# Optimization experiments

Measured on AMD Instinct MI355X. Metric: run time of the kernel, lower is better.

Reference implementation:

```python
import jax, jax.numpy as jnp
import numpy as np

WS = 7          # window_size
N = WS * WS     # 49 tokens per window
DIM = 384
H = 12
HD = DIM // H   # 32
NW = 64         # windows per image (mask leading dim)


def _rel_pos_index():
    coords = np.stack(np.meshgrid(np.arange(WS), np.arange(WS), indexing='ij'))  # (2, WS, WS)
    cf = coords.reshape(2, -1)                      # (2, N)
    rel = cf[:, :, None] - cf[:, None, :]           # (2, N, N)
    rel = rel.transpose(1, 2, 0)                    # (N, N, 2)
    idx = (rel[..., 0] + WS - 1) * (2 * WS - 1) + (rel[..., 1] + WS - 1)
    return jnp.asarray(idx, dtype=jnp.int32)        # (N, N)

REL_IDX = _rel_pos_index()


def setup_inputs() -> dict:
    key = jax.random.key(0)
    ks = jax.random.split(key, 10)
    B_ = 2048
    x = jax.random.normal(ks[0], (B_, N, DIM), dtype=jnp.float32)
    mask = jnp.zeros((NW, N, N), dtype=jnp.float32)
    s = 0.02
    Wq = jax.random.normal(ks[1], (DIM, DIM), jnp.float32) * s
    Wk = jax.random.normal(ks[2], (DIM, DIM), jnp.float32) * s
    Wv = jax.random.normal(ks[3], (DIM, DIM), jnp.float32) * s
    Wp = jax.random.normal(ks[4], (DIM, DIM), jnp.float32) * s
    bq = jnp.zeros((DIM,), jnp.float32)
    bk = jnp.zeros((DIM,), jnp.float32)
    bv = jnp.zeros((DIM,), jnp.float32)
    bp = jnp.zeros((DIM,), jnp.float32)
    table = jax.random.normal(ks[5], ((2 * WS - 1) ** 2, H), jnp.float32) * s
    return {"x": x, "mask": mask, "Wq": Wq, "bq": bq, "Wk": Wk, "bk": bk,
            "Wv": Wv, "bv": bv, "Wp": Wp, "bp": bp, "table": table}


def reference(x, mask, Wq, bq, Wk, bk, Wv, bv, Wp, bp, table):
    b_, n, c = x.shape
    scale = HD ** (-0.5)
    # projections: PyTorch Linear is x @ W.T + b
    q = (x @ Wq.T + bq).reshape(b_, n, H, HD).transpose(0, 2, 1, 3)  # (B, H, N, D)
    k = (x @ Wk.T + bk).reshape(b_, n, H, HD).transpose(0, 2, 1, 3)
    v = (x @ Wv.T + bv).reshape(b_, n, H, HD).transpose(0, 2, 1, 3)
    attn = jnp.einsum('bhnd,bhmd->bhnm', q * scale, k)               # (B, H, N, N)
    rel_bias = table[REL_IDX]                                        # (N, N, H)
    attn = attn + rel_bias.transpose(2, 0, 1)[None]                  # broadcast over B
    # mask add: (B//nW, nW, H, N, N) + mask[None, :, None]
    nw = mask.shape[0]
    attn = attn.reshape(b_ // nw, nw, H, n, n) + mask[None, :, None]
    attn = attn.reshape(b_, H, n, n)
    attn = jax.nn.softmax(attn, axis=-1)
    out = jnp.einsum('bhnm,bhmd->bhnd', attn, v)                     # (B, H, N, D)
    out = out.transpose(0, 2, 1, 3).reshape(b_, n, c)
    return out @ Wp.T + bp
```

## Files before the change

### kernel.cpp

```cpp
#include <hip/hip_runtime.h>
#include <stdint.h>

using bf16x8 = __attribute__((ext_vector_type(8))) short;
using f32x4  = __attribute__((ext_vector_type(4))) float;

__device__ __forceinline__ short f2bf(float f) {
  uint32_t u = __float_as_uint(f);
  u += 0x7fff + ((u >> 16) & 1u);
  return (short)(u >> 16);
}

#define MFMA16(a, b, c) __builtin_amdgcn_mfma_f32_16x16x32_bf16((a), (b), (c), 0, 0, 0)

__device__ __forceinline__ void gl_lds16(const short* g, short* l) {
  __builtin_amdgcn_global_load_lds(
      (const __attribute__((address_space(1))) void*)g,
      (__attribute__((address_space(3))) void*)l, 16, 0, 0);
}

__global__ void prep_w(const float* __restrict__ Wq, const float* __restrict__ bq,
                       const float* __restrict__ Wk, const float* __restrict__ bk,
                       const float* __restrict__ Wv, const float* __restrict__ bv,
                       const float* __restrict__ Wp, const float* __restrict__ bp,
                       short* __restrict__ Wqkv, short* __restrict__ Wpb,
                       float* __restrict__ bqkv, float* __restrict__ bpb) {
  int i = blockIdx.x * 256 + threadIdx.x;
  const float scale = 0.17677669529663687f;
  if (i < 1152 * 384) {
    int r = i / 384, k = i - r * 384;
    float v;
    if (r < 384)      v = Wq[r * 384 + k] * scale;
    else if (r < 768) v = Wk[(r - 384) * 384 + k];
    else              v = Wv[(r - 768) * 384 + k];
    Wqkv[i] = f2bf(v);
  }
  if (i < 384 * 384) Wpb[i] = f2bf(Wp[i]);
  if (i < 1152) bqkv[i] = (i < 384) ? bq[i] * scale : ((i < 768) ? bk[i - 384] : bv[i - 768]);
  if (i < 384) bpb[i] = bp[i];
}

__global__ void prep_bm(const float* __restrict__ table, const float* __restrict__ mask,
                        float* __restrict__ bmT, int nwmask) {
  int wm = blockIdx.x / 12, h = blockIdx.x - wm * 12;
  const float* mrow = mask + (size_t)wm * 2401;
  float* dst = bmT + (size_t)blockIdx.x * 4096;
  for (int e = threadIdx.x; e < 4096; e += 256) {
    int mn = e >> 8, cf = (e >> 4) & 15, if_ = e & 15;
    int row = (mn >> 2) * 16 + cf;
    int col = (mn & 3) * 16 + if_;
    float v = -3.0e38f;
    if (row < 49 && col < 49) {
      int id = row / 7, ir = row - id * 7;
      int jd = col / 7, jr = col - jd * 7;
      int idx = (id - jd + 6) * 13 + (ir - jr + 6);
      v = table[idx * 12 + h] + mrow[row * 49 + col];
    }
    dst[e] = v;
  }
}

__global__ void prep_x(const float* __restrict__ x, short* __restrict__ xb, int n8) {
  int u = blockIdx.x * 256 + threadIdx.x;
  if (u < n8) {
    int e = u * 8;
    float4 f0 = *(const float4*)(x + e);
    float4 f1 = *(const float4*)(x + e + 4);
    bf16x8 cv;
    cv[0] = f2bf(f0.x); cv[1] = f2bf(f0.y); cv[2] = f2bf(f0.z); cv[3] = f2bf(f0.w);
    cv[4] = f2bf(f1.x); cv[5] = f2bf(f1.y); cv[6] = f2bf(f1.z); cv[7] = f2bf(f1.w);
    *(bf16x8*)(xb + e) = cv;
  }
}

__global__ __launch_bounds__(256) void qkv_gemm(
    const short* __restrict__ xb, const short* __restrict__ Wqkv,
    const float* __restrict__ bqkv,
    short* __restrict__ qws, short* __restrict__ kws, short* __restrict__ vws,
    int ntok) {
  __shared__ __align__(16) short smem[2 * 320 * 64];
  const int tid = threadIdx.x;
  const int lane = tid & 63, wv = tid >> 6;
  const int c = lane & 15, g = lane >> 4;

  const int mt = gridDim.y;
  int id = blockIdx.y * 6 + blockIdx.x;
  int mt8 = mt & ~7;
  int xq, yq;
  if (id < 6 * mt8) {
    int q = id / 48, r = id - q * 48;
    yq = q * 8 + (r & 7);
    xq = r >> 3;
  } else {
    int rem = id - 6 * mt8;
    xq = rem % 6;
    yq = mt8 + rem / 6;
  }
  const int n0 = xq * 192;
  const int row0 = yq * 128;

  f32x4 acc[8][3];
  const f32x4 zero = {0.f, 0.f, 0.f, 0.f};
#pragma unroll
  for (int m = 0; m < 8; m++)
#pragma unroll
    for (int nn = 0; nn < 3; nn++) acc[m][nn] = zero;

  const int rsub = lane >> 3;
  const int chnk = ((lane & 7) ^ rsub) * 8;
  const short* aS[4];
  const short* bS[6];
#pragma unroll
  for (int i = 0; i < 4; i++) {
    int r = (wv * 4 + i) * 8 + rsub;
    int grow = row0 + r;
    if (grow >= ntok) grow = ntok - 1;
    aS[i] = xb + (size_t)grow * 384 + chnk;
  }
#pragma unroll
  for (int j = 0; j < 6; j++) {
    int r = (wv * 6 + j) * 8 + rsub;
    bS[j] = Wqkv + (size_t)(n0 + r) * 384 + chnk;
  }

  auto stage = [&](int buf, int ks) {
    short* Asl = smem + buf * (320 * 64);
    short* Bsl = Asl + 128 * 64;
#pragma unroll
    for (int i = 0; i < 4; i++)
      gl_lds16(aS[i] + ks * 64, Asl + (wv * 4 + i) * 512);
#pragma unroll
    for (int j = 0; j < 6; j++)
      gl_lds16(bS[j] + ks * 64, Bsl + (wv * 6 + j) * 512);
  };

  stage(0, 0);
  asm volatile("s_waitcnt vmcnt(0)" ::: "memory");
  __builtin_amdgcn_s_barrier();
#pragma unroll
  for (int ks = 0; ks < 6; ks++) {
    const int cur = ks & 1;
    if (ks < 5) {
      stage(cur ^ 1, ks + 1);
      asm volatile("s_waitcnt vmcnt(10)" ::: "memory");
    } else {
      asm volatile("s_waitcnt vmcnt(0)" ::: "memory");
    }
    __builtin_amdgcn_sched_barrier(0);
    __builtin_amdgcn_s_barrier();
    const short* Asl = smem + cur * (320 * 64);
    const short* Bsl = Asl + 128 * 64;
#pragma unroll
    for (int kk = 0; kk < 2; kk++) {
      bf16x8 af[8];
#pragma unroll
      for (int m = 0; m < 8; m++) {
        int row = m * 16 + c;
        af[m] = *(const bf16x8*)&Asl[row * 64 + (((kk * 4 + g) ^ (row & 7)) * 8)];
      }
#pragma unroll
      for (int nn = 0; nn < 3; nn++) {
        int row = wv * 48 + nn * 16 + c;
        bf16x8 bfr = *(const bf16x8*)&Bsl[row * 64 + (((kk * 4 + g) ^ (row & 7)) * 8)];
#pragma unroll
        for (int m = 0; m < 8; m++) acc[m][nn] = MFMA16(af[m], bfr, acc[m][nn]);
      }
    }
    __builtin_amdgcn_sched_barrier(0);
    __builtin_amdgcn_s_barrier();
  }

  const int s = n0 / 384;
  short* base = (s == 0) ? qws : ((s == 1) ? kws : vws);
  const int hbase = (n0 - s * 384) >> 5;
#pragma unroll
  for (int half = 0; half < 2; half++) {
    __syncthreads();
#pragma unroll
    for (int nn = 0; nn < 3; nn++) {
      int colRel = wv * 48 + nn * 16 + c;
      float bias = bqkv[n0 + colRel];
#pragma unroll
      for (int mm = 0; mm < 4; mm++) {
        int m = half * 4 + mm;
#pragma unroll
        for (int r = 0; r < 4; r++)
          smem[(mm * 16 + g * 4 + r) * 200 + colRel] = f2bf(acc[m][nn][r] + bias);
      }
    }
    __syncthreads();
    for (int u = tid; u < 384; u += 256) {
      int row = u & 63, j = u >> 6;
      int tr = row0 + half * 64 + row;
      if (tr < ntok) {
        int bw = tr / 49;
        int n = tr - bw * 49;
        short* dst = base + ((size_t)(bw * 12 + hbase + j) * 49 + n) * 32;
        const uint4* src = (const uint4*)&smem[row * 200 + j * 32];
        uint4* d4 = (uint4*)dst;
        d4[0] = src[0]; d4[1] = src[1]; d4[2] = src[2]; d4[3] = src[3];
      }
    }
  }
}

__global__ __launch_bounds__(256) void attn_kernel(
    const short* __restrict__ qws, const short* __restrict__ kws,
    const short* __restrict__ vws, short* __restrict__ ows,
    const float* __restrict__ bm, int b0, int nwmask) {
  __shared__ short Pall[4 * 64 * 72];
  const int tid = threadIdx.x;
  const int lane = tid & 63, wvi = tid >> 6;
  const int c = lane & 15, g = lane >> 4;
  const int task = blockIdx.x * 4 + wvi;
  const int b = task / 12, h = task - b * 12;
  const int wm = (b0 + b) % nwmask;
  const short* qb = qws + (size_t)(b * 12 + h) * 1568;
  const short* kb = kws + (size_t)(b * 12 + h) * 1568;
  const short* vb = vws + (size_t)(b * 12 + h) * 1568;

  bf16x8 qf[4], kf[4];
#pragma unroll
  for (int m = 0; m < 4; m++) { int i = m * 16 + c; if (i > 48) i = 48; qf[m] = *(const bf16x8*)(qb + i * 32 + g * 8); }
#pragma unroll
  for (int n = 0; n < 4; n++) { int j = n * 16 + c; if (j > 48) j = 48; kf[n] = *(const bf16x8*)(kb + j * 32 + g * 8); }

  bf16x8 vfr[2][2];
#pragma unroll
  for (int kk = 0; kk < 2; kk++)
#pragma unroll
    for (int dt = 0; dt < 2; dt++) {
      bf16x8 vf;
#pragma unroll
      for (int rr = 0; rr < 8; rr++) {
        int j = kk * 32 + g * 8 + rr; if (j > 48) j = 48;
        vf[rr] = vb[j * 32 + dt * 16 + c];
      }
      vfr[kk][dt] = vf;
    }

  const f32x4 zero = {0.f, 0.f, 0.f, 0.f};
  f32x4 S[4][4];
  __builtin_amdgcn_s_setprio(1);
#pragma unroll
  for (int m = 0; m < 4; m++)
#pragma unroll
    for (int n = 0; n < 4; n++) S[m][n] = MFMA16(kf[n], qf[m], zero);
  __builtin_amdgcn_s_setprio(0);

  const float* bmh = bm + (size_t)(wm * 12 + h) * 4096;
#pragma unroll
  for (int m = 0; m < 4; m++)
#pragma unroll
    for (int n = 0; n < 4; n++) {
      f32x4 b4 = *(const f32x4*)(bmh + ((m * 4 + n) * 16 + c) * 16 + g * 4);
      S[m][n][0] += b4[0]; S[m][n][1] += b4[1];
      S[m][n][2] += b4[2]; S[m][n][3] += b4[3];
    }

  short* P = Pall + wvi * 4608;
#pragma unroll
  for (int m = 0; m < 4; m++) {
    float mx = fmaxf(
        fmaxf(fmaxf(fmaxf(S[m][0][0], S[m][0][1]), fmaxf(S[m][0][2], S[m][0][3])),
              fmaxf(fmaxf(S[m][1][0], S[m][1][1]), fmaxf(S[m][1][2], S[m][1][3]))),
        fmaxf(fmaxf(fmaxf(S[m][2][0], S[m][2][1]), fmaxf(S[m][2][2], S[m][2][3])),
              fmaxf(fmaxf(S[m][3][0], S[m][3][1]), fmaxf(S[m][3][2], S[m][3][3]))));
    mx = fmaxf(mx, __shfl_xor(mx, 16));
    mx = fmaxf(mx, __shfl_xor(mx, 32));
    float e[4][4];
    float sm = 0.f;
#pragma unroll
    for (int n = 0; n < 4; n++)
#pragma unroll
      for (int r = 0; r < 4; r++) { e[n][r] = __expf(S[m][n][r] - mx); sm += e[n][r]; }
    sm += __shfl_xor(sm, 16);
    sm += __shfl_xor(sm, 32);
    float rv = 1.0f / sm;
#pragma unroll
    for (int n = 0; n < 4; n++) {
      uint32_t w0 = (uint32_t)(uint16_t)f2bf(e[n][0] * rv) |
                    ((uint32_t)(uint16_t)f2bf(e[n][1] * rv) << 16);
      uint32_t w1 = (uint32_t)(uint16_t)f2bf(e[n][2] * rv) |
                    ((uint32_t)(uint16_t)f2bf(e[n][3] * rv) << 16);
      uint2 w; w.x = w0; w.y = w1;
      *(uint2*)&P[(m * 16 + c) * 72 + n * 16 + g * 4] = w;
    }
  }

  f32x4 O[4][2];
#pragma unroll
  for (int m = 0; m < 4; m++) { O[m][0] = zero; O[m][1] = zero; }
#pragma unroll
  for (int kk = 0; kk < 2; kk++) {
    bf16x8 pf[4];
#pragma unroll
    for (int m = 0; m < 4; m++) pf[m] = *(const bf16x8*)&P[(m * 16 + c) * 72 + kk * 32 + g * 8];
    __builtin_amdgcn_s_setprio(1);
#pragma unroll
    for (int dt = 0; dt < 2; dt++)
#pragma unroll
      for (int m = 0; m < 4; m++) O[m][dt] = MFMA16(pf[m], vfr[kk][dt], O[m][dt]);
    __builtin_amdgcn_s_setprio(0);
  }
#pragma unroll
  for (int m = 0; m < 4; m++)
#pragma unroll
    for (int r = 0; r < 4; r++) {
      int i = m * 16 + g * 4 + r;
      if (i < 49) {
        size_t o = ((size_t)b * 49 + i) * 384 + h * 32;
        ows[o + c]      = f2bf(O[m][0][r]);
        ows[o + 16 + c] = f2bf(O[m][1][r]);
      }
    }
}

__global__ __launch_bounds__(256) void proj_gemm(
    const short* __restrict__ ows, const short* __restrict__ Wpb,
    const float* __restrict__ bpb, float* __restrict__ out,
    long tok0, int ntok) {
  __shared__ __align__(16) short smem[2 * 320 * 64];
  const int tid = threadIdx.x;
  const int lane = tid & 63, wv = tid >> 6;
  const int c = lane & 15, g = lane >> 4;

  const int mt = gridDim.y;
  int id = blockIdx.y * 2 + blockIdx.x;
  int mt8 = mt & ~7;
  int xq, yq;
  if (id < 2 * mt8) {
    int q = id / 16, r = id - q * 16;
    yq = q * 8 + (r & 7);
    xq = r >> 3;
  } else {
    int rem = id - 2 * mt8;
    xq = rem % 2;
    yq = mt8 + rem / 2;
  }
  const int n0 = xq * 192;
  const int row0 = yq * 128;

  f32x4 acc[8][3];
  const f32x4 zero = {0.f, 0.f, 0.f, 0.f};
#pragma unroll
  for (int m = 0; m < 8; m++)
#pragma unroll
    for (int nn = 0; nn < 3; nn++) acc[m][nn] = zero;

  const int rsub = lane >> 3;
  const int chnk = ((lane & 7) ^ rsub) * 8;
  const short* aS[4];
  const short* bS[6];
#pragma unroll
  for (int i = 0; i < 4; i++) {
    int r = (wv * 4 + i) * 8 + rsub;
    int grow = row0 + r;
    if (grow >= ntok) grow = ntok - 1;
    aS[i] = ows + (size_t)grow * 384 + chnk;
  }
#pragma unroll
  for (int j = 0; j < 6; j++) {
    int r = (wv * 6 + j) * 8 + rsub;
    bS[j] = Wpb + (size_t)(n0 + r) * 384 + chnk;
  }

  auto stage = [&](int buf, int ks) {
    short* Asl = smem + buf * (320 * 64);
    short* Bsl = Asl + 128 * 64;
#pragma unroll
    for (int i = 0; i < 4; i++)
      gl_lds16(aS[i] + ks * 64, Asl + (wv * 4 + i) * 512);
#pragma unroll
    for (int j = 0; j < 6; j++)
      gl_lds16(bS[j] + ks * 64, Bsl + (wv * 6 + j) * 512);
  };

  stage(0, 0);
  asm volatile("s_waitcnt vmcnt(0)" ::: "memory");
  __builtin_amdgcn_s_barrier();
#pragma unroll
  for (int ks = 0; ks < 6; ks++) {
    const int cur = ks & 1;
    if (ks < 5) {
      stage(cur ^ 1, ks + 1);
      asm volatile("s_waitcnt vmcnt(10)" ::: "memory");
    } else {
      asm volatile("s_waitcnt vmcnt(0)" ::: "memory");
    }
    __builtin_amdgcn_sched_barrier(0);
    __builtin_amdgcn_s_barrier();
    const short* Asl = smem + cur * (320 * 64);
    const short* Bsl = Asl + 128 * 64;
#pragma unroll
    for (int kk = 0; kk < 2; kk++) {
      bf16x8 af[8];
#pragma unroll
      for (int m = 0; m < 8; m++) {
        int row = m * 16 + c;
        af[m] = *(const bf16x8*)&Asl[row * 64 + (((kk * 4 + g) ^ (row & 7)) * 8)];
      }
#pragma unroll
      for (int nn = 0; nn < 3; nn++) {
        int row = wv * 48 + nn * 16 + c;
        bf16x8 bfr = *(const bf16x8*)&Bsl[row * 64 + (((kk * 4 + g) ^ (row & 7)) * 8)];
#pragma unroll
        for (int m = 0; m < 8; m++) acc[m][nn] = MFMA16(af[m], bfr, acc[m][nn]);
      }
    }
    __builtin_amdgcn_sched_barrier(0);
    __builtin_amdgcn_s_barrier();
  }

  float* fs = (float*)smem;
#pragma unroll
  for (int half = 0; half < 2; half++) {
    __syncthreads();
#pragma unroll
    for (int nn = 0; nn < 3; nn++) {
      int colRel = wv * 48 + nn * 16 + c;
      float bias = bpb[n0 + colRel];
#pragma unroll
      for (int mm = 0; mm < 4; mm++) {
        int m = half * 4 + mm;
#pragma unroll
        for (int r = 0; r < 4; r++)
          fs[(mm * 16 + g * 4 + r) * 196 + colRel] = acc[m][nn][r] + bias;
      }
    }
    __syncthreads();
#pragma unroll
    for (int t = 0; t < 12; t++) {
      int v = tid + t * 256;
      int row = v / 48, c4 = v - row * 48;
      int tr = row0 + half * 64 + row;
      if (tr < ntok)
        *(float4*)&out[(size_t)(tok0 + tr) * 384 + n0 + c4 * 4] =
            *(const float4*)&fs[row * 196 + c4 * 4];
    }
  }
}

extern "C" void kernel_launch(void* const* d_in, const int* in_sizes, int n_in,
                              void* d_out, int out_size, void* d_ws, size_t ws_size,
                              hipStream_t stream) {
  const float* x    = (const float*)d_in[0];
  const float* mask = (const float*)d_in[1];
  const float* Wq = (const float*)d_in[2];
  const float* bq = (const float*)d_in[3];
  const float* Wk = (const float*)d_in[4];
  const float* bk = (const float*)d_in[5];
  const float* Wv = (const float*)d_in[6];
  const float* bv = (const float*)d_in[7];
  const float* Wp = (const float*)d_in[8];
  const float* bp = (const float*)d_in[9];
  const float* table = (const float*)d_in[10];
  float* out = (float*)d_out;

  const int Btot = in_sizes[0] / (49 * 384);
  const int NWm  = in_sizes[1] / (49 * 49);

  char* ws = (char*)d_ws;
  short* Wqkv = (short*)ws;
  short* Wpb  = Wqkv + 1152 * 384;
  float* bqkv = (float*)(Wpb + 384 * 384);
  float* bpb  = bqkv + 1152;
  float* bmp  = bpb + 384;
  size_t fixedB = (size_t)(1152 * 384 + 384 * 384) * 2 + (1152 + 384) * 4
                + (size_t)NWm * 12 * 4096 * 4;
  char* dyn = ws + ((fixedB + 255) & ~(size_t)255);
  size_t used = (size_t)(dyn - ws);
  size_t avail = (ws_size > used + 4096) ? (ws_size - used - 4096) : 0;
  const size_t perw = (size_t)5 * 18816 * 2;
  long nwc = (long)(avail / perw);
  if (nwc > Btot) nwc = Btot;
  if (nwc >= 64) nwc &= ~63L;
  if (nwc < 1) nwc = 1;
  short* xbw = (short*)dyn;
  short* qws = xbw + (size_t)nwc * 18816;
  short* kws = qws + (size_t)nwc * 18816;
  short* vws = kws + (size_t)nwc * 18816;
  short* ows = vws + (size_t)nwc * 18816;

  prep_w<<<dim3(1728), dim3(256), 0, stream>>>(Wq, bq, Wk, bk, Wv, bv, Wp, bp,
                                               Wqkv, Wpb, bqkv, bpb);
  prep_bm<<<dim3(NWm * 12), dim3(256), 0, stream>>>(table, mask, bmp, NWm);

  for (long b0 = 0; b0 < Btot; b0 += nwc) {
    int nw = (int)((Btot - b0 < nwc) ? (Btot - b0) : nwc);
    int ntok = nw * 49;
    long tok0 = b0 * 49;
    int n8 = ntok * 48;
    prep_x<<<dim3((n8 + 255) / 256), dim3(256), 0, stream>>>(x + tok0 * 384, xbw, n8);
    int mt = (ntok + 127) / 128;
    qkv_gemm<<<dim3(6, mt), dim3(256), 0, stream>>>(xbw, Wqkv, bqkv, qws, kws, vws, ntok);
    attn_kernel<<<dim3(3 * nw), dim3(256), 0, stream>>>(qws, kws, vws, ows, bmp,
                                                        (int)b0, NWm);
    proj_gemm<<<dim3(2, mt), dim3(256), 0, stream>>>(ows, Wpb, bpb, out, tok0, ntok);
  }
}
```

Before: 543.8 us.

## Halve GEMM K-tile to shrink LDS and convert prep_x to grid-stride loop

Both qkv and proj GEMMs now stage 32-wide K slices instead of 64, halving LDS use per block (so more blocks can be resident per CU), with a 4-chunk XOR swizzle and twelve pipeline steps instead of six. The proj epilogue is split into four quarter passes so its staging fits the smaller LDS. prep_x becomes a grid-stride loop with a capped grid. The tradeoff is more barriers and wait points per K step, with less MFMA work between them to hide load latency.

```diff
diff --git a/kernel.cpp b/kernel.cpp
--- a/kernel.cpp
+++ b/kernel.cpp
@@ -60,8 +60,7 @@
 }
 
 __global__ void prep_x(const float* __restrict__ x, short* __restrict__ xb, int n8) {
-  int u = blockIdx.x * 256 + threadIdx.x;
-  if (u < n8) {
+  for (int u = blockIdx.x * 256 + threadIdx.x; u < n8; u += gridDim.x * 256) {
     int e = u * 8;
     float4 f0 = *(const float4*)(x + e);
     float4 f1 = *(const float4*)(x + e + 4);
@@ -77,10 +76,11 @@
     const float* __restrict__ bqkv,
     short* __restrict__ qws, short* __restrict__ kws, short* __restrict__ vws,
     int ntok) {
-  __shared__ __align__(16) short smem[2 * 320 * 64];
+  __shared__ __align__(16) short smem[2 * 320 * 32];
   const int tid = threadIdx.x;
   const int lane = tid & 63, wv = tid >> 6;
   const int c = lane & 15, g = lane >> 4;
+  const int cx = c & 3;
 
   const int mt = gridDim.y;
   int id = blockIdx.y * 6 + blockIdx.x;
@@ -105,65 +105,62 @@
 #pragma unroll
     for (int nn = 0; nn < 3; nn++) acc[m][nn] = zero;
 
-  const int rsub = lane >> 3;
-  const int chnk = ((lane & 7) ^ rsub) * 8;
-  const short* aS[4];
-  const short* bS[6];
-#pragma unroll
-  for (int i = 0; i < 4; i++) {
-    int r = (wv * 4 + i) * 8 + rsub;
-    int grow = row0 + r;
+  const int r4 = lane >> 2;
+  const int schnk = ((lane & 3) ^ (r4 & 3)) * 8;
+  const short* aS[2];
+  const short* bS[3];
+#pragma unroll
+  for (int i = 0; i < 2; i++) {
+    int rl = (wv * 2 + i) * 16 + r4;
+    int grow = row0 + rl;
     if (grow >= ntok) grow = ntok - 1;
-    aS[i] = xb + (size_t)grow * 384 + chnk;
-  }
-#pragma unroll
-  for (int j = 0; j < 6; j++) {
-    int r = (wv * 6 + j) * 8 + rsub;
-    bS[j] = Wqkv + (size_t)(n0 + r) * 384 + chnk;
+    aS[i] = xb + (size_t)grow * 384 + schnk;
+  }
+#pragma unroll
+  for (int j = 0; j < 3; j++) {
+    int rl = (wv * 3 + j) * 16 + r4;
+    bS[j] = Wqkv + (size_t)(n0 + rl) * 384 + schnk;
   }
 
   auto stage = [&](int buf, int ks) {
-    short* Asl = smem + buf * (320 * 64);
-    short* Bsl = Asl + 128 * 64;
-#pragma unroll
-    for (int i = 0; i < 4; i++)
-      gl_lds16(aS[i] + ks * 64, Asl + (wv * 4 + i) * 512);
-#pragma unroll
-    for (int j = 0; j < 6; j++)
-      gl_lds16(bS[j] + ks * 64, Bsl + (wv * 6 + j) * 512);
+    short* Asl = smem + buf * (320 * 32);
+    short* Bsl = Asl + 128 * 32;
+#pragma unroll
+    for (int i = 0; i < 2; i++)
+      gl_lds16(aS[i] + ks * 32, Asl + (wv * 2 + i) * 512);
+#pragma unroll
+    for (int j = 0; j < 3; j++)
+      gl_lds16(bS[j] + ks * 32, Bsl + (wv * 3 + j) * 512);
   };
 
   stage(0, 0);
   asm volatile("s_waitcnt vmcnt(0)" ::: "memory");
   __builtin_amdgcn_s_barrier();
 #pragma unroll
-  for (int ks = 0; ks < 6; ks++) {
+  for (int ks = 0; ks < 12; ks++) {
     const int cur = ks & 1;
-    if (ks < 5) {
+    if (ks < 11) {
       stage(cur ^ 1, ks + 1);
-      asm volatile("s_waitcnt vmcnt(10)" ::: "memory");
+      asm volatile("s_waitcnt vmcnt(5)" ::: "memory");
     } else {
       asm volatile("s_waitcnt vmcnt(0)" ::: "memory");
     }
     __builtin_amdgcn_sched_barrier(0);
     __builtin_amdgcn_s_barrier();
-    const short* Asl = smem + cur * (320 * 64);
-    const short* Bsl = Asl + 128 * 64;
-#pragma unroll
-    for (int kk = 0; kk < 2; kk++) {
-      bf16x8 af[8];
-#pragma unroll
-      for (int m = 0; m < 8; m++) {
-        int row = m * 16 + c;
-        af[m] = *(const bf16x8*)&Asl[row * 64 + (((kk * 4 + g) ^ (row & 7)) * 8)];
-      }
-#pragma unroll
-      for (int nn = 0; nn < 3; nn++) {
-        int row = wv * 48 + nn * 16 + c;
-        bf16x8 bfr = *(const bf16x8*)&Bsl[row * 64 + (((kk * 4 + g) ^ (row & 7)) * 8)];
-#pragma unroll
-        for (int m = 0; m < 8; m++) acc[m][nn] = MFMA16(af[m], bfr, acc[m][nn]);
-      }
+    const short* Asl = smem + cur * (320 * 32);
+    const short* Bsl = Asl + 128 * 32;
+    bf16x8 af[8];
+#pragma unroll
+    for (int m = 0; m < 8; m++) {
+      int row = m * 16 + c;
+      af[m] = *(const bf16x8*)&Asl[row * 32 + ((g ^ cx) * 8)];
+    }
+#pragma unroll
+    for (int nn = 0; nn < 3; nn++) {
+      int row = wv * 48 + nn * 16 + c;
+      bf16x8 bfr = *(const bf16x8*)&Bsl[row * 32 + ((g ^ cx) * 8)];
+#pragma unroll
+      for (int m = 0; m < 8; m++) acc[m][nn] = MFMA16(af[m], bfr, acc[m][nn]);
     }
     __builtin_amdgcn_sched_barrier(0);
     __builtin_amdgcn_s_barrier();
@@ -319,10 +316,11 @@
     const short* __restrict__ ows, const short* __restrict__ Wpb,
     const float* __restrict__ bpb, float* __restrict__ out,
     long tok0, int ntok) {
-  __shared__ __align__(16) short smem[2 * 320 * 64];
+  __shared__ __align__(16) short smem[2 * 320 * 32];
   const int tid = threadIdx.x;
   const int lane = tid & 63, wv = tid >> 6;
   const int c = lane & 15, g = lane >> 4;
+  const int cx = c & 3;
 
   const int mt = gridDim.y;
   int id = blockIdx.y * 2 + blockIdx.x;
@@ -347,65 +345,62 @@
 #pragma unroll
     for (int nn = 0; nn < 3; nn++) acc[m][nn] = zero;
 
-  const int rsub = lane >> 3;
-  const int chnk = ((lane & 7) ^ rsub) * 8;
-  const short* aS[4];
-  const short* bS[6];
-#pragma unroll
-  for (int i = 0; i < 4; i++) {
-    int r = (wv * 4 + i) * 8 + rsub;
-    int grow = row0 + r;
+  const int r4 = lane >> 2;
+  const int schnk = ((lane & 3) ^ (r4 & 3)) * 8;
+  const short* aS[2];
+  const short* bS[3];
+#pragma unroll
+  for (int i = 0; i < 2; i++) {
+    int rl = (wv * 2 + i) * 16 + r4;
+    int grow = row0 + rl;
     if (grow >= ntok) grow = ntok - 1;
-    aS[i] = ows + (size_t)grow * 384 + chnk;
-  }
-#pragma unroll
-  for (int j = 0; j < 6; j++) {
-    int r = (wv * 6 + j) * 8 + rsub;
-    bS[j] = Wpb + (size_t)(n0 + r) * 384 + chnk;
+    aS[i] = ows + (size_t)grow * 384 + schnk;
+  }
+#pragma unroll
+  for (int j = 0; j < 3; j++) {
+    int rl = (wv * 3 + j) * 16 + r4;
+    bS[j] = Wpb + (size_t)(n0 + rl) * 384 + schnk;
   }
 
   auto stage = [&](int buf, int ks) {
-    short* Asl = smem + buf * (320 * 64);
-    short* Bsl = Asl + 128 * 64;
-#pragma unroll
-    for (int i = 0; i < 4; i++)
-      gl_lds16(aS[i] + ks * 64, Asl + (wv * 4 + i) * 512);
-#pragma unroll
-    for (int j = 0; j < 6; j++)
-      gl_lds16(bS[j] + ks * 64, Bsl + (wv * 6 + j) * 512);
+    short* Asl = smem + buf * (320 * 32);
+    short* Bsl = Asl + 128 * 32;
+#pragma unroll
+    for (int i = 0; i < 2; i++)
+      gl_lds16(aS[i] + ks * 32, Asl + (wv * 2 + i) * 512);
+#pragma unroll
+    for (int j = 0; j < 3; j++)
+      gl_lds16(bS[j] + ks * 32, Bsl + (wv * 3 + j) * 512);
   };
 
   stage(0, 0);
   asm volatile("s_waitcnt vmcnt(0)" ::: "memory");
   __builtin_amdgcn_s_barrier();
 #pragma unroll
-  for (int ks = 0; ks < 6; ks++) {
+  for (int ks = 0; ks < 12; ks++) {
     const int cur = ks & 1;
-    if (ks < 5) {
+    if (ks < 11) {
       stage(cur ^ 1, ks + 1);
-      asm volatile("s_waitcnt vmcnt(10)" ::: "memory");
+      asm volatile("s_waitcnt vmcnt(5)" ::: "memory");
     } else {
       asm volatile("s_waitcnt vmcnt(0)" ::: "memory");
     }
     __builtin_amdgcn_sched_barrier(0);
     __builtin_amdgcn_s_barrier();
-    const short* Asl = smem + cur * (320 * 64);
-    const short* Bsl = Asl + 128 * 64;
-#pragma unroll
-    for (int kk = 0; kk < 2; kk++) {
-      bf16x8 af[8];
-#pragma unroll
-      for (int m = 0; m < 8; m++) {
-        int row = m * 16 + c;
-        af[m] = *(const bf16x8*)&Asl[row * 64 + (((kk * 4 + g) ^ (row & 7)) * 8)];
-      }
-#pragma unroll
-      for (int nn = 0; nn < 3; nn++) {
-        int row = wv * 48 + nn * 16 + c;
-        bf16x8 bfr = *(const bf16x8*)&Bsl[row * 64 + (((kk * 4 + g) ^ (row & 7)) * 8)];
-#pragma unroll
-        for (int m = 0; m < 8; m++) acc[m][nn] = MFMA16(af[m], bfr, acc[m][nn]);
-      }
+    const short* Asl = smem + cur * (320 * 32);
+    const short* Bsl = Asl + 128 * 32;
+    bf16x8 af[8];
+#pragma unroll
+    for (int m = 0; m < 8; m++) {
+      int row = m * 16 + c;
+      af[m] = *(const bf16x8*)&Asl[row * 32 + ((g ^ cx) * 8)];
+    }
+#pragma unroll
+    for (int nn = 0; nn < 3; nn++) {
+      int row = wv * 48 + nn * 16 + c;
+      bf16x8 bfr = *(const bf16x8*)&Bsl[row * 32 + ((g ^ cx) * 8)];
+#pragma unroll
+      for (int m = 0; m < 8; m++) acc[m][nn] = MFMA16(af[m], bfr, acc[m][nn]);
     }
     __builtin_amdgcn_sched_barrier(0);
     __builtin_amdgcn_s_barrier();
@@ -413,15 +408,15 @@
 
   float* fs = (float*)smem;
 #pragma unroll
-  for (int half = 0; half < 2; half++) {
+  for (int qtr = 0; qtr < 4; qtr++) {
     __syncthreads();
 #pragma unroll
     for (int nn = 0; nn < 3; nn++) {
       int colRel = wv * 48 + nn * 16 + c;
       float bias = bpb[n0 + colRel];
 #pragma unroll
-      for (int mm = 0; mm < 4; mm++) {
-        int m = half * 4 + mm;
+      for (int mm = 0; mm < 2; mm++) {
+        int m = qtr * 2 + mm;
 #pragma unroll
         for (int r = 0; r < 4; r++)
           fs[(mm * 16 + g * 4 + r) * 196 + colRel] = acc[m][nn][r] + bias;
@@ -429,10 +424,10 @@
     }
     __syncthreads();
 #pragma unroll
-    for (int t = 0; t < 12; t++) {
+    for (int t = 0; t < 6; t++) {
       int v = tid + t * 256;
       int row = v / 48, c4 = v - row * 48;
-      int tr = row0 + half * 64 + row;
+      int tr = row0 + qtr * 32 + row;
       if (tr < ntok)
         *(float4*)&out[(size_t)(tok0 + tr) * 384 + n0 + c4 * 4] =
             *(const float4*)&fs[row * 196 + c4 * 4];
@@ -490,7 +485,8 @@
     int ntok = nw * 49;
     long tok0 = b0 * 49;
     int n8 = ntok * 48;
-    prep_x<<<dim3((n8 + 255) / 256), dim3(256), 0, stream>>>(x + tok0 * 384, xbw, n8);
+    int pxb = (n8 + 255) / 256; if (pxb > 2048) pxb = 2048;
+    prep_x<<<dim3(pxb), dim3(256), 0, stream>>>(x + tok0 * 384, xbw, n8);
     int mt = (ntok + 127) / 128;
     qkv_gemm<<<dim3(6, mt), dim3(256), 0, stream>>>(xbw, Wqkv, bqkv, qws, kws, vws, ntok);
     attn_kernel<<<dim3(3 * nw), dim3(256), 0, stream>>>(qws, kws, vws, ows, bmp,
```

Measured after the change: 571.8 us. 5.1% more time.
